# Kernel tuning notes

Measured on AMD Instinct MI355X. Metric: run time of the kernel, lower is better.

Reference implementation:

```python
import jax, jax.numpy as jnp
import numpy as np

IN_DIM = 64
OUT_DIM = 64
BN_EPS = 1e-5


def setup_inputs() -> dict:
    key = jax.random.key(0)
    ks = jax.random.split(key, 8)
    B, N, D, O = 8, 512, IN_DIM, OUT_DIM
    s_in = 1.0 / np.sqrt(D)
    x = jax.random.normal(ks[0], (B, N, D), dtype=jnp.float32)
    # torch Linear weights stored as (in, out) so forward is x @ W + b
    W_ap = jax.random.uniform(ks[1], (D, O), jnp.float32, -s_in, s_in)
    b_ap = jnp.zeros((O,), jnp.float32)
    att_w = jax.random.normal(ks[2], (O, 1), jnp.float32) * np.sqrt(2.0 / (O + 1))  # xavier_normal_
    W_pa = jax.random.uniform(ks[3], (D, O), jnp.float32, -s_in, s_in)
    b_pa = jnp.zeros((O,), jnp.float32)
    W_po = jax.random.uniform(ks[4], (D, O), jnp.float32, -s_in, s_in)
    b_po = jnp.zeros((O,), jnp.float32)
    gamma = jnp.ones((O,), jnp.float32)
    beta = jnp.zeros((O,), jnp.float32)
    run_mean = jnp.zeros((O,), jnp.float32)
    run_var = jnp.ones((O,), jnp.float32)
    return {"x": x, "W_ap": W_ap, "b_ap": b_ap, "att_w": att_w,
            "W_pa": W_pa, "b_pa": b_pa, "W_po": W_po, "b_po": b_po,
            "gamma": gamma, "beta": beta, "run_mean": run_mean, "run_var": run_var}


def reference(x, W_ap, b_ap, att_w, W_pa, b_pa, W_po, b_po, gamma, beta, run_mean, run_var):
    # GraphAttentionLayer forward (eval mode: dropout = identity, BN uses running stats)
    # pairwise multiplication of nodes: (b, n, n, d)
    pair = x[:, :, None, :] * x[:, None, :, :]
    # per-pair attention projection + tanh: (b, n, n, o)
    att = jnp.tanh(jnp.einsum('bijd,do->bijo', pair, W_ap) + b_ap)
    # attention-weight vector -> scalar score per pair: (b, n, n, 1)
    scores = att @ att_w
    # softmax over the second node axis (dim=-2 in torch)
    att_map = jax.nn.softmax(scores, axis=-2)[..., 0]  # (b, n, n)
    # attention-weighted aggregation + projections
    agg = jnp.einsum('bij,bjd->bid', att_map, x)
    h = agg @ W_pa + b_pa + (x @ W_po + b_po)
    # BatchNorm1d in inference form
    h = (h - run_mean) * jax.lax.rsqrt(run_var + BN_EPS) * gamma + beta
    return jax.nn.selu(h)
```

## Files before the change

kernel.cpp:

```cpp
#include <hip/hip_runtime.h>
#include <cstdint>

typedef __attribute__((ext_vector_type(8))) short bf16x8;
typedef __attribute__((ext_vector_type(4))) float f32x4;

#if __has_builtin(__builtin_amdgcn_exp2f)
#define EXP2F(x) __builtin_amdgcn_exp2f(x)
#else
#define EXP2F(x) exp2f(x)
#endif
#if __has_builtin(__builtin_amdgcn_rcpf)
#define RCPF(x) __builtin_amdgcn_rcpf(x)
#else
#define RCPF(x) (1.0f/(x))
#endif

#define C2LOG2E 2.885390081777927f
#define LOG2E   1.4426950408889634f

__device__ __forceinline__ unsigned int f2bf(float f) {
    union { float f; unsigned int u; } v; v.f = f;
    return ((v.u + 0x7FFFu + ((v.u >> 16) & 1u)) >> 16);
}
__device__ __forceinline__ float bf2f(unsigned short h) {
    union { unsigned int u; float f; } v; v.u = ((unsigned int)h) << 16; return v.f;
}

__global__ void prep_kernel(const float* __restrict__ x, const float* __restrict__ W_ap,
                            const float* __restrict__ W_pa, const float* __restrict__ W_po,
                            const float* __restrict__ b_pa, const float* __restrict__ b_po,
                            const float* __restrict__ gma, const float* __restrict__ bta,
                            const float* __restrict__ rmean, const float* __restrict__ rvar,
                            unsigned short* __restrict__ Xb, unsigned short* __restrict__ XT,
                            float* __restrict__ Wt,
                            unsigned short* __restrict__ Wpab, unsigned short* __restrict__ Wpob,
                            float* __restrict__ bnA, float* __restrict__ bnBB) {
    int t = blockIdx.x * 256 + threadIdx.x;
    const float* src = x + (size_t)t * 8;
    float4 a = *(const float4*)(src);
    float4 b = *(const float4*)(src + 4);
    unsigned int p0 = f2bf(a.x) | (f2bf(a.y) << 16);
    unsigned int p1 = f2bf(a.z) | (f2bf(a.w) << 16);
    unsigned int p2 = f2bf(b.x) | (f2bf(b.y) << 16);
    unsigned int p3 = f2bf(b.z) | (f2bf(b.w) << 16);
    *(int4*)(Xb + (size_t)t * 8) = make_int4((int)p0, (int)p1, (int)p2, (int)p3);
    {
        int bb = t >> 12;
        int bj = (t >> 3) & 511;
        int d0 = (t & 7) * 8;
        unsigned short* xt = XT + (size_t)bb * (64 * 512) + bj;
        unsigned short e[8] = {(unsigned short)(p0 & 0xffff), (unsigned short)(p0 >> 16),
                               (unsigned short)(p1 & 0xffff), (unsigned short)(p1 >> 16),
                               (unsigned short)(p2 & 0xffff), (unsigned short)(p2 >> 16),
                               (unsigned short)(p3 & 0xffff), (unsigned short)(p3 >> 16)};
        #pragma unroll
        for (int k = 0; k < 8; ++k) xt[(size_t)(d0 + k) * 512] = e[k];
    }
    if (t < 64 * 64) {
        int src_i = (t & 63) * 64 + (t >> 6);
        Wt[t]   = W_ap[src_i];
        Wpab[t] = (unsigned short)f2bf(W_pa[src_i]);
        Wpob[t] = (unsigned short)f2bf(W_po[src_i]);
    }
    if (t < 64) {
        float A = gma[t] * rsqrtf(rvar[t] + 1e-5f);
        bnA[t]  = A;
        bnBB[t] = (b_pa[t] + b_po[t] - rmean[t]) * A + bta[t];
    }
}

__global__ __launch_bounds__(1024, 1) void score_kernel(
    const float* __restrict__ x, const float* __restrict__ b_ap, const float* __restrict__ att_w,
    const unsigned short* __restrict__ Xb, const float* __restrict__ Wt,
    unsigned short* __restrict__ E)
{
    __shared__ unsigned short stage[17][16][16];

    const int t  = threadIdx.x;
    const int l  = t & 63;
    const int w  = t >> 6;
    const int bid = blockIdx.x;
    const int b   = bid & 7;
    const int strip = bid >> 3;
    const int i0  = strip * 16;
    const int i   = i0 + w;
    const int lm = l & 15;
    const int lq = l >> 4;
    const unsigned short* __restrict__ Xg = Xb + (size_t)b * (512 * 64);
    const float* __restrict__ xi = x + ((size_t)b * 512 + i) * 64;

    bf16x8 af[8];
    #pragma unroll
    for (int ks = 0; ks < 2; ++ks) {
        float4 xc0 = *(const float4*)(xi + ks * 32 + lq * 8);
        float4 xc1 = *(const float4*)(xi + ks * 32 + lq * 8 + 4);
        xc0.x *= C2LOG2E; xc0.y *= C2LOG2E; xc0.z *= C2LOG2E; xc0.w *= C2LOG2E;
        xc1.x *= C2LOG2E; xc1.y *= C2LOG2E; xc1.z *= C2LOG2E; xc1.w *= C2LOG2E;
        #pragma unroll
        for (int of = 0; of < 4; ++of) {
            const float* wr = Wt + (of * 16 + lm) * 64 + ks * 32 + lq * 8;
            float4 w0 = *(const float4*)(wr);
            float4 w1 = *(const float4*)(wr + 4);
            unsigned int p0 = f2bf(w0.x * xc0.x) | (f2bf(w0.y * xc0.y) << 16);
            unsigned int p1 = f2bf(w0.z * xc0.z) | (f2bf(w0.w * xc0.w) << 16);
            unsigned int p2 = f2bf(w1.x * xc1.x) | (f2bf(w1.y * xc1.y) << 16);
            unsigned int p3 = f2bf(w1.z * xc1.z) | (f2bf(w1.w * xc1.w) << 16);
            int4 pk = make_int4((int)p0, (int)p1, (int)p2, (int)p3);
            af[of * 2 + ks] = *reinterpret_cast<bf16x8*>(&pk);
        }
    }

    float n2a[16];
    f32x4 binit[4];
    float asum = 0.f, aabs = 0.f;
    #pragma unroll
    for (int of = 0; of < 4; ++of) {
        #pragma unroll
        for (int r = 0; r < 4; ++r) {
            int o = of * 16 + lq * 4 + r;
            float a = att_w[o];
            n2a[of * 4 + r] = -2.f * a;
            binit[of][r]    = C2LOG2E * b_ap[o];
            asum += a;
            aabs += fabsf(a);
        }
    }
    asum += __shfl_xor(asum, 16); asum += __shfl_xor(asum, 32);
    aabs += __shfl_xor(aabs, 16); aabs += __shfl_xor(aabs, 32);
    const float coff = (asum - aabs) * LOG2E;

    const int smax = (strip < 16) ? 17 : 16;
    unsigned short* __restrict__ Erow = E + ((size_t)b * 512 + i) * 512;
    unsigned short* __restrict__ Ecb  = E + (size_t)b * (512 * 512);
    const unsigned short* xrow = Xg + lm * 64 + lq * 8;

    for (int s = 0; s < smax; ++s) {
        const int jt = (strip + s) & 31;
        bf16x8 b0 = *(const bf16x8*)(xrow + jt * 1024);
        bf16x8 b1 = *(const bf16x8*)(xrow + jt * 1024 + 32);
        f32x4 a0 = binit[0], a1 = binit[1], a2 = binit[2], a3 = binit[3];
        a0 = __builtin_amdgcn_mfma_f32_16x16x32_bf16(af[0], b0, a0, 0, 0, 0);
        a1 = __builtin_amdgcn_mfma_f32_16x16x32_bf16(af[2], b0, a1, 0, 0, 0);
        a2 = __builtin_amdgcn_mfma_f32_16x16x32_bf16(af[4], b0, a2, 0, 0, 0);
        a3 = __builtin_amdgcn_mfma_f32_16x16x32_bf16(af[6], b0, a3, 0, 0, 0);
        a0 = __builtin_amdgcn_mfma_f32_16x16x32_bf16(af[1], b1, a0, 0, 0, 0);
        a1 = __builtin_amdgcn_mfma_f32_16x16x32_bf16(af[3], b1, a1, 0, 0, 0);
        a2 = __builtin_amdgcn_mfma_f32_16x16x32_bf16(af[5], b1, a2, 0, 0, 0);
        a3 = __builtin_amdgcn_mfma_f32_16x16x32_bf16(af[7], b1, a3, 0, 0, 0);
        float ex[16], tt[16];
        #pragma unroll
        for (int r = 0; r < 4; ++r) {
            ex[r]      = EXP2F(a0[r]);
            ex[4 + r]  = EXP2F(a1[r]);
            ex[8 + r]  = EXP2F(a2[r]);
            ex[12 + r] = EXP2F(a3[r]);
        }
        #pragma unroll
        for (int k = 0; k < 16; ++k) tt[k] = RCPF(1.f + ex[k]);
        float q0 = 0.f, q1 = 0.f, q2 = 0.f, q3 = 0.f;
        #pragma unroll
        for (int r = 0; r < 4; ++r) {
            q0 = fmaf(n2a[r],      tt[r],      q0);
            q1 = fmaf(n2a[4 + r],  tt[4 + r],  q1);
            q2 = fmaf(n2a[8 + r],  tt[8 + r],  q2);
            q3 = fmaf(n2a[12 + r], tt[12 + r], q3);
        }
        float ss = (q0 + q1) + (q2 + q3);
        ss += __shfl_xor(ss, 16);
        ss += __shfl_xor(ss, 32);
        float ee = EXP2F(fmaf(ss, LOG2E, coff));
        unsigned short eb = (unsigned short)f2bf(ee);
        if (l < 16) {
            Erow[jt * 16 + l] = eb;
            stage[s][l][w] = eb;
        }
    }
    __syncthreads();

    const int nm = smax - 1;
    if (t < nm * 16) {
        int si = 1 + (t >> 4);
        int jl = t & 15;
        int jt = (strip + si) & 31;
        const unsigned short* sp = &stage[si][jl][0];
        int4 v0 = *(const int4*)(sp);
        int4 v1 = *(const int4*)(sp + 8);
        unsigned short* dst = Ecb + (size_t)(jt * 16 + jl) * 512 + i0;
        *(int4*)(dst)     = v0;
        *(int4*)(dst + 8) = v1;
    }
}

__global__ __launch_bounds__(256, 4) void agg_kernel(
    const unsigned short* __restrict__ Xb, const unsigned short* __restrict__ XT,
    const unsigned short* __restrict__ E,
    const unsigned short* __restrict__ Wpab, const unsigned short* __restrict__ Wpob,
    const float* __restrict__ bnA, const float* __restrict__ bnBB,
    float* __restrict__ out)
{
    __shared__ float sInv[16];
    __shared__ unsigned short pA[16][72];

    const int t  = threadIdx.x;
    const int l  = t & 63;
    const int w  = t >> 6;
    const int bid = blockIdx.x;
    const int b   = bid & 7;
    const int i0  = (bid >> 3) * 16;
    const int lm = l & 15;
    const int lq = l >> 4;

    const unsigned short* Erow  = E  + ((size_t)b * 512 + i0 + lm) * 512 + lq * 8;
    const unsigned short* xtrow = XT + (size_t)b * (64 * 512) + (w * 16 + lm) * 512 + lq * 8;
    f32x4 acc = (f32x4){0.f, 0.f, 0.f, 0.f};
    float den = 0.f;
    #pragma unroll
    for (int jc = 0; jc < 16; ++jc) {
        bf16x8 ae = *(const bf16x8*)(Erow + jc * 32);
        bf16x8 bx = *(const bf16x8*)(xtrow + jc * 32);
        acc = __builtin_amdgcn_mfma_f32_16x16x32_bf16(ae, bx, acc, 0, 0, 0);
        if (w == 0) {
            #pragma unroll
            for (int e = 0; e < 8; ++e) den += bf2f((unsigned short)ae[e]);
        }
    }
    if (w == 0) {
        den += __shfl_xor(den, 16);
        den += __shfl_xor(den, 32);
        if (l < 16) sInv[l] = RCPF(den);
    }
    #pragma unroll
    for (int r = 0; r < 4; ++r)
        pA[lq * 4 + r][w * 16 + lm] = (unsigned short)f2bf(acc[r]);
    __syncthreads();

    bf16x8 af2[2], afx[2], bwa[2], bwo[2];
    #pragma unroll
    for (int kc = 0; kc < 2; ++kc) {
        af2[kc] = *(const bf16x8*)(&pA[lm][kc * 32 + lq * 8]);
        afx[kc] = *(const bf16x8*)(Xb + ((size_t)b * 512 + i0 + lm) * 64 + kc * 32 + lq * 8);
        bwa[kc] = *(const bf16x8*)(Wpab + (w * 16 + lm) * 64 + kc * 32 + lq * 8);
        bwo[kc] = *(const bf16x8*)(Wpob + (w * 16 + lm) * 64 + kc * 32 + lq * 8);
    }
    f32x4 a2a = (f32x4){0.f, 0.f, 0.f, 0.f};
    f32x4 a2x = (f32x4){0.f, 0.f, 0.f, 0.f};
    a2a = __builtin_amdgcn_mfma_f32_16x16x32_bf16(af2[0], bwa[0], a2a, 0, 0, 0);
    a2x = __builtin_amdgcn_mfma_f32_16x16x32_bf16(afx[0], bwo[0], a2x, 0, 0, 0);
    a2a = __builtin_amdgcn_mfma_f32_16x16x32_bf16(af2[1], bwa[1], a2a, 0, 0, 0);
    a2x = __builtin_amdgcn_mfma_f32_16x16x32_bf16(afx[1], bwo[1], a2x, 0, 0, 0);

    const int o = w * 16 + lm;
    const float A  = bnA[o];
    const float BB = bnBB[o];
    const float alpha = 1.6732632423543772f, scale = 1.0507009873554805f;
    #pragma unroll
    for (int r = 0; r < 4; ++r) {
        int i = i0 + lq * 4 + r;
        float hv = fmaf(sInv[lq * 4 + r], a2a[r], a2x[r]);
        hv = fmaf(hv, A, BB);
        float neg = alpha * (EXP2F(hv * LOG2E) - 1.0f);
        out[((size_t)b * 512 + i) * 64 + o] = scale * (hv > 0.f ? hv : neg);
    }
}

extern "C" void kernel_launch(void* const* d_in, const int* in_sizes, int n_in,
                              void* d_out, int out_size, void* d_ws, size_t ws_size,
                              hipStream_t stream) {
    const float* x     = (const float*)d_in[0];
    const float* W_ap  = (const float*)d_in[1];
    const float* b_ap  = (const float*)d_in[2];
    const float* att_w = (const float*)d_in[3];
    const float* W_pa  = (const float*)d_in[4];
    const float* b_pa  = (const float*)d_in[5];
    const float* W_po  = (const float*)d_in[6];
    const float* b_po  = (const float*)d_in[7];
    const float* gma   = (const float*)d_in[8];
    const float* bta   = (const float*)d_in[9];
    const float* rmean = (const float*)d_in[10];
    const float* rvar  = (const float*)d_in[11];

    char* ws = (char*)d_ws;
    unsigned short* Xb   = (unsigned short*)ws;
    unsigned short* XT   = (unsigned short*)(ws + 512 * 1024);
    float* Wt            = (float*)(ws + 1024 * 1024);
    unsigned short* Wpab = (unsigned short*)(ws + 1040 * 1024);
    unsigned short* Wpob = (unsigned short*)(ws + 1048 * 1024);
    float* bnA           = (float*)(ws + 1056 * 1024);
    float* bnBB          = (float*)(ws + 1057 * 1024);
    unsigned short* E    = (unsigned short*)(ws + 1088 * 1024);
    float* out           = (float*)d_out;

    prep_kernel<<<128, 256, 0, stream>>>(x, W_ap, W_pa, W_po, b_pa, b_po, gma, bta,
                                         rmean, rvar, Xb, XT, Wt, Wpab, Wpob, bnA, bnBB);
    score_kernel<<<256, 1024, 0, stream>>>(x, b_ap, att_w, Xb, Wt, E);
    agg_kernel<<<256, 256, 0, stream>>>(Xb, XT, E, Wpab, Wpob, bnA, bnBB, out);
}
```

Baseline: 45.15 us.

## Write mirrored score tiles to a tiled buffer and transpose XT via LDS

The score kernel's symmetric mirrored tiles were scattered as 32-byte chunks into strided rows of E. They now go contiguously into a separate tiled buffer M, and the aggregation kernel picks per 16-column group whether to read from E or M. The prep kernel also builds the transposed bf16 X through shared memory, so it writes whole 16-byte vectors instead of scattered 2-byte stores. This trades strided global writes for extra address logic and a data-dependent choice of load source in the aggregation inner loop.

Result: no change. 45.18 us, median of 2 (+0.1%).

```diff
diff --git a/kernel.cpp b/kernel.cpp
--- a/kernel.cpp
+++ b/kernel.cpp
@@ -35,6 +35,7 @@
                             float* __restrict__ Wt,
                             unsigned short* __restrict__ Wpab, unsigned short* __restrict__ Wpob,
                             float* __restrict__ bnA, float* __restrict__ bnBB) {
+    __shared__ unsigned short sx[64][40];
     int t = blockIdx.x * 256 + threadIdx.x;
     const float* src = x + (size_t)t * 8;
     float4 a = *(const float4*)(src);
@@ -45,16 +46,20 @@
     unsigned int p3 = f2bf(b.z) | (f2bf(b.w) << 16);
     *(int4*)(Xb + (size_t)t * 8) = make_int4((int)p0, (int)p1, (int)p2, (int)p3);
     {
-        int bb = t >> 12;
-        int bj = (t >> 3) & 511;
-        int d0 = (t & 7) * 8;
-        unsigned short* xt = XT + (size_t)bb * (64 * 512) + bj;
-        unsigned short e[8] = {(unsigned short)(p0 & 0xffff), (unsigned short)(p0 >> 16),
-                               (unsigned short)(p1 & 0xffff), (unsigned short)(p1 >> 16),
-                               (unsigned short)(p2 & 0xffff), (unsigned short)(p2 >> 16),
-                               (unsigned short)(p3 & 0xffff), (unsigned short)(p3 >> 16)};
-        #pragma unroll
-        for (int k = 0; k < 8; ++k) xt[(size_t)(d0 + k) * 512] = e[k];
+        int tl = threadIdx.x;
+        int jloc = tl >> 3, d0 = (tl & 7) * 8;
+        unsigned short e8[8] = {(unsigned short)(p0 & 0xffff), (unsigned short)(p0 >> 16),
+                                (unsigned short)(p1 & 0xffff), (unsigned short)(p1 >> 16),
+                                (unsigned short)(p2 & 0xffff), (unsigned short)(p2 >> 16),
+                                (unsigned short)(p3 & 0xffff), (unsigned short)(p3 >> 16)};
+        #pragma unroll
+        for (int e = 0; e < 8; ++e) sx[d0 + e][jloc] = e8[e];
+        __syncthreads();
+        int bb  = blockIdx.x >> 4;
+        int jr0 = (blockIdx.x & 15) * 32;
+        int d   = tl >> 2, jo = (tl & 3) * 8;
+        int4 v = *(const int4*)(&sx[d][jo]);
+        *(int4*)(XT + (size_t)bb * (64 * 512) + (size_t)d * 512 + jr0 + jo) = v;
     }
     if (t < 64 * 64) {
         int src_i = (t & 63) * 64 + (t >> 6);
@@ -72,7 +77,7 @@
 __global__ __launch_bounds__(1024, 1) void score_kernel(
     const float* __restrict__ x, const float* __restrict__ b_ap, const float* __restrict__ att_w,
     const unsigned short* __restrict__ Xb, const float* __restrict__ Wt,
-    unsigned short* __restrict__ E)
+    unsigned short* __restrict__ E, unsigned short* __restrict__ M)
 {
     __shared__ unsigned short stage[17][16][16];
 
@@ -131,7 +136,6 @@
 
     const int smax = (strip < 16) ? 17 : 16;
     unsigned short* __restrict__ Erow = E + ((size_t)b * 512 + i) * 512;
-    unsigned short* __restrict__ Ecb  = E + (size_t)b * (512 * 512);
     const unsigned short* xrow = Xg + lm * 64 + lq * 8;
 
     for (int s = 0; s < smax; ++s) {
@@ -181,11 +185,10 @@
     if (t < nm * 16) {
         int si = 1 + (t >> 4);
         int jl = t & 15;
-        int jt = (strip + si) & 31;
         const unsigned short* sp = &stage[si][jl][0];
         int4 v0 = *(const int4*)(sp);
         int4 v1 = *(const int4*)(sp + 8);
-        unsigned short* dst = Ecb + (size_t)(jt * 16 + jl) * 512 + i0;
+        unsigned short* dst = M + ((((size_t)(b * 32 + strip) * 16) + (si - 1)) * 16 + jl) * 16;
         *(int4*)(dst)     = v0;
         *(int4*)(dst + 8) = v1;
     }
@@ -193,7 +196,7 @@
 
 __global__ __launch_bounds__(256, 4) void agg_kernel(
     const unsigned short* __restrict__ Xb, const unsigned short* __restrict__ XT,
-    const unsigned short* __restrict__ E,
+    const unsigned short* __restrict__ E, const unsigned short* __restrict__ M,
     const unsigned short* __restrict__ Wpab, const unsigned short* __restrict__ Wpob,
     const float* __restrict__ bnA, const float* __restrict__ bnBB,
     float* __restrict__ out)
@@ -209,14 +212,23 @@
     const int i0  = (bid >> 3) * 16;
     const int lm = l & 15;
     const int lq = l >> 4;
-
-    const unsigned short* Erow  = E  + ((size_t)b * 512 + i0 + lm) * 512 + lq * 8;
+    const int Sr = i0 >> 4;
+    const int smax_r = (Sr < 16) ? 17 : 16;
+
+    const unsigned short* Ebase = E + ((size_t)b * 512 + i0 + lm) * 512 + (lq & 1) * 8;
+    const unsigned short* Mbase = M + (size_t)b * (32 * 16 * 16 * 16) + lm * 16 + (lq & 1) * 8;
     const unsigned short* xtrow = XT + (size_t)b * (64 * 512) + (w * 16 + lm) * 512 + lq * 8;
     f32x4 acc = (f32x4){0.f, 0.f, 0.f, 0.f};
     float den = 0.f;
     #pragma unroll
     for (int jc = 0; jc < 16; ++jc) {
-        bf16x8 ae = *(const bf16x8*)(Erow + jc * 32);
+        int g   = 2 * jc + (lq >> 1);
+        int del = (g - Sr) & 31;
+        int s   = (Sr - g) & 31;
+        const unsigned short* pa = (del < smax_r)
+            ? Ebase + g * 16
+            : Mbase + (((size_t)g * 16) + (s - 1)) * 256;
+        bf16x8 ae = *(const bf16x8*)pa;
         bf16x8 bx = *(const bf16x8*)(xtrow + jc * 32);
         acc = __builtin_amdgcn_mfma_f32_16x16x32_bf16(ae, bx, acc, 0, 0, 0);
         if (w == 0) {
@@ -288,10 +300,11 @@
     float* bnA           = (float*)(ws + 1056 * 1024);
     float* bnBB          = (float*)(ws + 1057 * 1024);
     unsigned short* E    = (unsigned short*)(ws + 1088 * 1024);
+    unsigned short* M    = (unsigned short*)(ws + 5184 * 1024);
     float* out           = (float*)d_out;
 
     prep_kernel<<<128, 256, 0, stream>>>(x, W_ap, W_pa, W_po, b_pa, b_po, gma, bta,
                                          rmean, rvar, Xb, XT, Wt, Wpab, Wpob, bnA, bnBB);
-    score_kernel<<<256, 1024, 0, stream>>>(x, b_ap, att_w, Xb, Wt, E);
-    agg_kernel<<<256, 256, 0, stream>>>(Xb, XT, E, Wpab, Wpob, bnA, bnBB, out);
-}
+    score_kernel<<<256, 1024, 0, stream>>>(x, b_ap, att_w, Xb, Wt, E, M);
+    agg_kernel<<<256, 256, 0, stream>>>(Xb, XT, E, M, Wpab, Wpob, bnA, bnBB, out);
+}
```
